# Optimization experiments

Hardware: AMD Instinct MI355X
Metric: run time of the kernel (lower is better)

Reference implementation:

```python
import jax, jax.numpy as jnp
import numpy as np

B, T, IN_DIM = 64, 128, 64
T_ENC, HID, ATTN, OUT = 256, 512, 256, 64


def setup_inputs() -> dict:
    key = jax.random.key(0)
    ks = jax.random.split(key, 12)
    s = lambda *sh: 1.0 / np.sqrt(sh[-1])
    inp = {
        "x": jax.random.normal(ks[0], (B, T, IN_DIM), jnp.float32),
        "encoder_outputs": jax.random.normal(ks[1], (B, T_ENC, HID), jnp.float32),
        # Bahdanau attention params (Linear, no bias): weight shape (out, in)
        "W_query": jax.random.normal(ks[2], (ATTN, HID), jnp.float32) * s(ATTN, HID),
        "W_key": jax.random.normal(ks[3], (ATTN, HID), jnp.float32) * s(ATTN, HID),
        "v": jax.random.normal(ks[4], (1, ATTN), jnp.float32) * s(1, ATTN),
        # LSTM params, PyTorch layout: gates order (i, f, g, o), 4H rows
        "W_ih": jax.random.normal(ks[5], (4 * HID, IN_DIM + HID), jnp.float32) * s(1, HID),
        "W_hh": jax.random.normal(ks[6], (4 * HID, HID), jnp.float32) * s(1, HID),
        "b_ih": jax.random.normal(ks[7], (4 * HID,), jnp.float32) * s(1, HID),
        "b_hh": jax.random.normal(ks[8], (4 * HID,), jnp.float32) * s(1, HID),
        # FC output layer
        "W_fc": jax.random.normal(ks[9], (OUT, HID), jnp.float32) * s(1, HID),
        "b_fc": jax.random.normal(ks[10], (OUT,), jnp.float32) * s(1, HID),
    }
    return inp


def reference(x, encoder_outputs, W_query, W_key, v, W_ih, W_hh, b_ih, b_hh, W_fc, b_fc):
    Bsz = x.shape[0]
    H = W_hh.shape[1]
    # keys projection is constant across timesteps -> hoist out of the loop
    keys_t = jnp.einsum('bed,ad->bea', encoder_outputs, W_key)  # (B, T_enc, A)
    bias = b_ih + b_hh

    def step(carry, x_t):
        h, c = carry  # (B, H) each
        # Bahdanau attention: query = previous top-layer hidden state
        q = jnp.einsum('bh,ah->ba', h, W_query)                 # (B, A)
        energy = jnp.tanh(q[:, None, :] + keys_t)               # (B, T_enc, A)
        e = jnp.einsum('bea,a->be', energy, v[0])               # (B, T_enc)
        w = jax.nn.softmax(e, axis=1)                           # (B, T_enc)
        context = jnp.einsum('be,bed->bd', w, encoder_outputs)  # (B, H)
        # single-step LSTM
        inp = jnp.concatenate([x_t, context], axis=-1)          # (B, IN+H)
        gates = inp @ W_ih.T + h @ W_hh.T + bias                # (B, 4H)
        i_g, f_g, g_g, o_g = jnp.split(gates, 4, axis=-1)
        c_new = jax.nn.sigmoid(f_g) * c + jax.nn.sigmoid(i_g) * jnp.tanh(g_g)
        h_new = jax.nn.sigmoid(o_g) * jnp.tanh(c_new)
        out_t = h_new @ W_fc.T + b_fc                           # (B, OUT)
        return (h_new, c_new), out_t

    h0 = jnp.zeros((Bsz, H), x.dtype)
    c0 = jnp.zeros((Bsz, H), x.dtype)
    _, outs = jax.lax.scan(step, (h0, c0), jnp.swapaxes(x, 0, 1))  # (T, B, OUT)
    return jnp.swapaxes(outs, 0, 1)  # (B, T, OUT)
```

## Files before the change

kernel.cpp:

```cpp
#include <hip/hip_runtime.h>


#define B 64
#define T 128
#define IN_DIM 64
#define TE 256
#define HID 512
#define ATTN 256
#define OUTD 64
#define G 256
#define BS 512

typedef __attribute__((ext_vector_type(8))) short short8;
typedef __attribute__((ext_vector_type(4))) float f32x4;

__device__ __forceinline__ float fast_exp(float x) {
  return __builtin_amdgcn_exp2f(x * 1.44269504f);
}
__device__ __forceinline__ float fast_tanh(float x) {
  float ax = fabsf(x);
  float z = __builtin_amdgcn_exp2f(ax * -2.885390082f);
  float r = (1.f - z) * __builtin_amdgcn_rcpf(1.f + z);
  return copysignf(r, x);
}
__device__ __forceinline__ float fast_sig(float x) {
  float z = __builtin_amdgcn_exp2f(x * -1.44269504f);
  return __builtin_amdgcn_rcpf(1.f + z);
}
__device__ __forceinline__ float bfu(unsigned short u) {
  return __uint_as_float((unsigned)u << 16);
}
__device__ __forceinline__ float bflo(unsigned u) { return __uint_as_float(u << 16); }
__device__ __forceinline__ float bfhi(unsigned u) {
  return __uint_as_float(u & 0xffff0000u);
}
__device__ __forceinline__ unsigned f2bf(float f) {
  unsigned u = __float_as_uint(f);
  return (u + 0x7fff + ((u >> 16) & 1)) >> 16;
}

__device__ __forceinline__ float ald(const float* p) {
  return __hip_atomic_load((float*)p, __ATOMIC_RELAXED, __HIP_MEMORY_SCOPE_AGENT);
}
__device__ __forceinline__ float2 ald2(const float* p) {
  double d = __hip_atomic_load((const double*)p, __ATOMIC_RELAXED,
                               __HIP_MEMORY_SCOPE_AGENT);
  union { double d; float2 f; } u; u.d = d; return u.f;
}
__device__ __forceinline__ unsigned aldu(const unsigned* p) {
  return __hip_atomic_load(p, __ATOMIC_RELAXED, __HIP_MEMORY_SCOPE_AGENT);
}
__device__ __forceinline__ void ast(float* p, float v) {
  __hip_atomic_store(p, v, __ATOMIC_RELAXED, __HIP_MEMORY_SCOPE_AGENT);
}
__device__ __forceinline__ void astu(unsigned* p, unsigned v) {
  __hip_atomic_store(p, v, __ATOMIC_RELAXED, __HIP_MEMORY_SCOPE_AGENT);
}

__device__ __forceinline__ void gridbar(int* flags, int seq, int bid, int tid) {
  asm volatile("s_waitcnt vmcnt(0)" ::: "memory");
  __syncthreads();
  if (tid == 0)
    __hip_atomic_store(&flags[bid], seq, __ATOMIC_RELAXED, __HIP_MEMORY_SCOPE_AGENT);
  if (tid < 64) {
    int* fb = flags + (bid & ~63);
    while (__hip_atomic_load(&fb[tid], __ATOMIC_RELAXED,
                             __HIP_MEMORY_SCOPE_AGENT) < seq) {
      __builtin_amdgcn_s_sleep(1);
    }
  }
  __syncthreads();
}

__global__ void cvt_kernel(const float* __restrict__ src,
                           unsigned short* __restrict__ dst, int n) {
  for (int i = blockIdx.x * blockDim.x + threadIdx.x; i < n;
       i += gridDim.x * blockDim.x)
    dst[i] = (unsigned short)f2bf(src[i]);
}
__global__ void pack2_kernel(const float* __restrict__ src,
                             unsigned* __restrict__ dst, int n2) {
  for (int i = blockIdx.x * blockDim.x + threadIdx.x; i < n2;
       i += gridDim.x * blockDim.x)
    dst[i] = f2bf(src[2 * i]) | (f2bf(src[2 * i + 1]) << 16);
}

__global__ __launch_bounds__(256, 2) void keys_kernel(
    const float* __restrict__ enc, const float* __restrict__ Wk,
    unsigned short* __restrict__ keys2) {
  __shared__ float et[16][512];
  __shared__ float wk[32][256];
  const int tid = threadIdx.x;
  const int b = blockIdx.x >> 4;
  const int e0 = (blockIdx.x & 15) * 16;

  for (int p = 0; p < 8; ++p) {
    int i = p * 256 + tid;
    int e = i >> 7, kq = i & 127;
    float4 vv = *(const float4*)&enc[((size_t)(b * TE + e0 + e)) * HID + kq * 4];
    *(float4*)&et[e][kq * 4] = vv;
  }

  float acc[8][2];
  #pragma unroll
  for (int i = 0; i < 8; ++i) { acc[i][0] = 0.f; acc[i][1] = 0.f; }
  const int a0 = tid & 127;
  const int eh = (tid >> 7) * 8;

  for (int kc = 0; kc < 512; kc += 32) {
    __syncthreads();
    for (int p = 0; p < 8; ++p) {
      int i = p * 256 + tid;
      int a = i >> 3, j4 = (i & 7) * 4;
      float4 w4 = *(const float4*)&Wk[(size_t)a * HID + kc + j4];
      wk[j4 + 0][a] = w4.x; wk[j4 + 1][a] = w4.y;
      wk[j4 + 2][a] = w4.z; wk[j4 + 3][a] = w4.w;
    }
    __syncthreads();
    for (int k = 0; k < 32; ++k) {
      float w0 = wk[k][a0], w1 = wk[k][a0 + 128];
      #pragma unroll
      for (int i = 0; i < 8; ++i) {
        float ev = et[eh + i][kc + k];
        acc[i][0] = fmaf(ev, w0, acc[i][0]);
        acc[i][1] = fmaf(ev, w1, acc[i][1]);
      }
    }
  }
  #pragma unroll
  for (int i = 0; i < 8; ++i)
    #pragma unroll
    for (int h = 0; h < 2; ++h)
      keys2[((size_t)(b * TE + e0 + eh + i)) * ATTN + a0 + 128 * h] =
          (unsigned short)f2bf(acc[i][h]);
}

__global__ __launch_bounds__(BS, 2) void main_kernel(
    const float* __restrict__ v,
    const float* __restrict__ Wih, const float* __restrict__ Whh,
    const float* __restrict__ bih, const float* __restrict__ bhh,
    const float* __restrict__ bfc,
    const unsigned short* __restrict__ enc2, const unsigned short* __restrict__ keys2,
    const unsigned short* __restrict__ Wq2, const unsigned short* __restrict__ Wfc2,
    const unsigned* __restrict__ x2pk,
    float* hbuf, float* cbuf, float* ctxb, float* denb, unsigned* hpk,
    int* flags, float* out) {
  const int bid = blockIdx.x, tid = threadIdx.x;
  const int g = bid >> 6, idx = bid & 63;
  const int b = g * 16 + (idx >> 2), qt = idx & 3;
  const int rg = idx, bg = g;
  const int lane = tid & 63, wv = tid >> 6;

  __shared__ unsigned alds[34 * 256];
  __shared__ float pc[2 * 4 * 16 * 17];
  __shared__ float glds[16 * 33];
  __shared__ float hsh[HID];
  __shared__ float qsh[320];
  __shared__ float lwsh[64];
  __shared__ float dsh[16];
  __shared__ float blds[32];

  if (tid < 32) {
    const int gr2 = (tid >> 3) * 512 + rg * 8 + (tid & 7);
    blds[tid] = bih[gr2] + bhh[gr2];
  }
  const float4 vvf = *(const float4*)&v[lane * 4];
  float kkf[8][4];
  #pragma unroll
  for (int i = 0; i < 8; ++i) {
    const unsigned short* kr =
        keys2 + ((size_t)(b * TE) + qt * 64 + wv * 8 + i) * ATTN + lane * 4;
    uint2 k4 = *(const uint2*)kr;
    kkf[i][0] = bflo(k4.x); kkf[i][1] = bfhi(k4.x);
    kkf[i][2] = bflo(k4.y); kkf[i][3] = bfhi(k4.y);
  }
  const int mL = lane & 15, qL = lane >> 4;
  const int nt = wv >> 2, kq = wv & 3;
  const int kstart = (kq < 2) ? kq * 9 : 18 + (kq - 2) * 8;
  const int nch = (kq < 2) ? 9 : 8;
  const int aoff = mL * 16 + ((qL * 4) ^ (((mL >> 1) & 3) * 4));
  short8 bh[9], bl[9];
  {
    const int rloc = nt * 16 + mL;
    const int grow2 = (rloc >> 3) * 512 + rg * 8 + (rloc & 7);
    #pragma unroll
    for (int c = 0; c < 9; ++c) {
      unsigned uh[4] = {0, 0, 0, 0}, ul[4] = {0, 0, 0, 0};
      if (c < nch) {
        const int kc = kstart + c;
        #pragma unroll
        for (int j = 0; j < 8; ++j) {
          const int k = kc * 32 + qL * 8 + j;
          const float w = (k < 576) ? Wih[(size_t)grow2 * 576 + k]
                                    : Whh[(size_t)grow2 * 512 + (k - 576)];
          const unsigned hi = f2bf(w);
          const float lo = w - __uint_as_float(hi << 16);
          uh[j >> 1] |= hi << (16 * (j & 1));
          ul[j >> 1] |= f2bf(lo) << (16 * (j & 1));
        }
      }
      uint4 th; th.x = uh[0]; th.y = uh[1]; th.z = uh[2]; th.w = uh[3];
      uint4 tl; tl.x = ul[0]; tl.y = ul[1]; tl.z = ul[2]; tl.w = ul[3];
      bh[c] = __builtin_bit_cast(short8, th);
      bl[c] = __builtin_bit_cast(short8, tl);
    }
  }

  const int sm = tid >> 5, ss = tid & 31;
  const int bgl = bg * 16 + sm;
  const int dcol = (ss & 15) ^ (((sm >> 1) & 3) * 4);

  int seq = 0;

  for (int t = 0; t < T; ++t) {
    {
      const float* hprev = hbuf + (size_t)(t & 1) * B * HID;
      hsh[tid] = ald(hprev + (size_t)b * HID + tid);
      {
        unsigned pkx = x2pk[((size_t)bgl * T + t) * 32 + ss];
        const unsigned* hpkc = hpk + (size_t)(t & 1) * B * 256 + (size_t)bgl * 256;
        unsigned ph[8];
        #pragma unroll
        for (int p = 0; p < 8; ++p) ph[p] = aldu(hpkc + ss + 32 * p);
        alds[(ss >> 4) * 256 + sm * 16 + dcol] = pkx;
        #pragma unroll
        for (int p = 0; p < 8; ++p) {
          const int i = ss + 32 * (p + 9);
          alds[(i >> 4) * 256 + sm * 16 + dcol] = ph[p];
        }
      }
      __syncthreads();
      if (t >= 1 && tid < 128) {
        const int o = qt * 16 + (tid >> 3), c = tid & 7;
        const unsigned short* wr = Wfc2 + (size_t)o * HID;
        float oa = 0.f;
        #pragma unroll
        for (int j = 0; j < 8; ++j) {
          const int jj = c * 64 + ((j + c) & 7) * 8;
          uint4 w8 = *(const uint4*)(wr + jj);
          const float* hp = &hsh[jj];
          oa = fmaf(bflo(w8.x), hp[0], oa); oa = fmaf(bfhi(w8.x), hp[1], oa);
          oa = fmaf(bflo(w8.y), hp[2], oa); oa = fmaf(bfhi(w8.y), hp[3], oa);
          oa = fmaf(bflo(w8.z), hp[4], oa); oa = fmaf(bfhi(w8.z), hp[5], oa);
          oa = fmaf(bflo(w8.w), hp[6], oa); oa = fmaf(bfhi(w8.w), hp[7], oa);
        }
        oa += __shfl_xor(oa, 1, 64); oa += __shfl_xor(oa, 2, 64);
        oa += __shfl_xor(oa, 4, 64);
        if (c == 0) out[((size_t)b * T + (t - 1)) * OUTD + o] = oa + bfc[o];
      }
      {
        const int r = tid >> 1, c2 = tid & 1;
        const unsigned short* wr = Wq2 + (size_t)r * HID + c2 * 256;
        const float* hb = &hsh[c2 * 256];
        float qa0 = 0.f, qa1 = 0.f;
        #pragma unroll 8
        for (int j = 0; j < 32; ++j) {
          uint4 w8 = ((const uint4*)wr)[j];
          const float* hp = hb + j * 8;
          qa0 = fmaf(bflo(w8.x), hp[0], qa0); qa0 = fmaf(bfhi(w8.x), hp[1], qa0);
          qa0 = fmaf(bflo(w8.y), hp[2], qa0); qa0 = fmaf(bfhi(w8.y), hp[3], qa0);
          qa1 = fmaf(bflo(w8.z), hp[4], qa1); qa1 = fmaf(bfhi(w8.z), hp[5], qa1);
          qa1 = fmaf(bflo(w8.w), hp[6], qa1); qa1 = fmaf(bfhi(w8.w), hp[7], qa1);
        }
        float qa = qa0 + qa1;
        qa += __shfl_xor(qa, 1, 64);
        if (c2 == 0) qsh[r + (r >> 2)] = qa;
      }
      __syncthreads();
      {
        float q4[4];
        #pragma unroll
        for (int j = 0; j < 4; ++j) q4[j] = qsh[5 * lane + j];
        #pragma unroll
        for (int i = 0; i < 8; ++i) {
          float p = fast_tanh(q4[0] + kkf[i][0]) * vvf.x;
          p = fmaf(fast_tanh(q4[1] + kkf[i][1]), vvf.y, p);
          p = fmaf(fast_tanh(q4[2] + kkf[i][2]), vvf.z, p);
          p = fmaf(fast_tanh(q4[3] + kkf[i][3]), vvf.w, p);
          #pragma unroll
          for (int m = 1; m < 64; m <<= 1) p += __shfl_xor(p, m, 64);
          if (lane == 0) lwsh[wv * 8 + i] = fast_exp(p);
        }
      }
      __syncthreads();
      if (tid < 64) {
        float p = lwsh[tid];
        #pragma unroll
        for (int m = 1; m < 64; m <<= 1) p += __shfl_xor(p, m, 64);
        if (tid == 0) atomicAdd(denb + (t & 1) * B + b, p);
      }
      if (tid < 128)
        ast(ctxb + (size_t)((t + 1) & 1) * B * HID + b * HID + qt * 128 + tid, 0.f);
      if (qt == 0 && tid == 0) ast(denb + ((t + 1) & 1) * B + b, 0.f);
      {
        const unsigned short* erow = enc2 + ((size_t)(b * TE) + qt * 64) * HID + tid;
        float a0 = 0.f, a1 = 0.f, a2 = 0.f, a3 = 0.f;
        #pragma unroll
        for (int e = 0; e < 64; e += 4) {
          a0 = fmaf(lwsh[e],     bfu(erow[(size_t)e * HID]),       a0);
          a1 = fmaf(lwsh[e + 1], bfu(erow[(size_t)(e + 1) * HID]), a1);
          a2 = fmaf(lwsh[e + 2], bfu(erow[(size_t)(e + 2) * HID]), a2);
          a3 = fmaf(lwsh[e + 3], bfu(erow[(size_t)(e + 3) * HID]), a3);
        }
        atomicAdd(ctxb + (size_t)(t & 1) * B * HID + b * HID + tid,
                  (a0 + a1) + (a2 + a3));
      }
    }
    ++seq; gridbar(flags, seq, bid, tid);

    {
      float* hnext = hbuf + (size_t)((t + 1) & 1) * B * HID;
      const float* ctxcur = ctxb + (size_t)(t & 1) * B * HID;
      if (tid < 16) dsh[tid] = ald(denb + (t & 1) * B + bg * 16 + tid);
      float2 cv[8];
      #pragma unroll
      for (int p = 0; p < 8; ++p)
        cv[p] = ald2(ctxcur + (size_t)bgl * HID + (2 * (ss + 32 * (p + 1)) - 64));
      __syncthreads();
      {
        const float li = __builtin_amdgcn_rcpf(dsh[sm]);
        #pragma unroll
        for (int p = 0; p < 8; ++p) {
          const int i = ss + 32 * (p + 1);
          unsigned pk = f2bf(cv[p].x * li) | (f2bf(cv[p].y * li) << 16);
          alds[(i >> 4) * 256 + sm * 16 + dcol] = pk;
        }
      }
      __syncthreads();
      {
        f32x4 ach = {0.f, 0.f, 0.f, 0.f}, acl = {0.f, 0.f, 0.f, 0.f};
        #pragma unroll
        for (int c = 0; c < 9; ++c) {
          if (c < nch) {
            const uint4 av = *(const uint4*)&alds[(kstart + c) * 256 + aoff];
            const short8 a8 = __builtin_bit_cast(short8, av);
            ach = __builtin_amdgcn_mfma_f32_16x16x32_bf16(a8, bh[c], ach, 0, 0, 0);
            acl = __builtin_amdgcn_mfma_f32_16x16x32_bf16(a8, bl[c], acl, 0, 0, 0);
          }
        }
        #pragma unroll
        for (int rr = 0; rr < 4; ++rr)
          pc[((nt * 4 + kq) * 16 + qL * 4 + rr) * 17 + mL] = ach[rr] + acl[rr];
      }
      __syncthreads();
      {
        const int r2 = tid >> 4, mb = tid & 15;
        const int pbase = ((r2 >> 4) * 64 + mb) * 17 + (r2 & 15);
        float s = blds[r2] + ((pc[pbase] + pc[pbase + 272]) +
                              (pc[pbase + 544] + pc[pbase + 816]));
        glds[mb * 33 + r2] = s;
      }
      __syncthreads();
      if (tid < 128) {
        const int bbl = tid >> 3, hl = tid & 7;
        const int bb2 = bg * 16 + bbl, hu = rg * 8 + hl;
        const float gi = glds[bbl * 33 + hl],      gf = glds[bbl * 33 + 8 + hl];
        const float gg = glds[bbl * 33 + 16 + hl], go = glds[bbl * 33 + 24 + hl];
        const float cold = cbuf[bb2 * HID + hu];
        const float cn = fast_sig(gf) * cold + fast_sig(gi) * fast_tanh(gg);
        const float hn = fast_sig(go) * fast_tanh(cn);
        cbuf[bb2 * HID + hu] = cn;
        ast(&hnext[bb2 * HID + hu], hn);
        const float ho = __shfl_xor(hn, 1, 64);
        if ((hl & 1) == 0)
          astu(hpk + (size_t)((t + 1) & 1) * B * 256 + bb2 * 256 + rg * 4 + (hl >> 1),
               f2bf(hn) | (f2bf(ho) << 16));
      }
    }
    ++seq; gridbar(flags, seq, bid, tid);
  }

  {
    hsh[tid] = ald(hbuf + (size_t)b * HID + tid);
    __syncthreads();
    if (tid < 128) {
      const int o = qt * 16 + (tid >> 3), c = tid & 7;
      const unsigned short* wr = Wfc2 + (size_t)o * HID;
      float oa = 0.f;
      #pragma unroll
      for (int j = 0; j < 8; ++j) {
        const int jj = c * 64 + ((j + c) & 7) * 8;
        uint4 w8 = *(const uint4*)(wr + jj);
        const float* hp = &hsh[jj];
        oa = fmaf(bflo(w8.x), hp[0], oa); oa = fmaf(bfhi(w8.x), hp[1], oa);
        oa = fmaf(bflo(w8.y), hp[2], oa); oa = fmaf(bfhi(w8.y), hp[3], oa);
        oa = fmaf(bflo(w8.z), hp[4], oa); oa = fmaf(bfhi(w8.z), hp[5], oa);
        oa = fmaf(bflo(w8.w), hp[6], oa); oa = fmaf(bfhi(w8.w), hp[7], oa);
      }
      oa += __shfl_xor(oa, 1, 64); oa += __shfl_xor(oa, 2, 64);
      oa += __shfl_xor(oa, 4, 64);
      if (c == 0) out[((size_t)b * T + 127) * OUTD + o] = oa + bfc[o];
    }
  }
}

extern "C" void kernel_launch(void* const* d_in, const int* in_sizes, int n_in,
                              void* d_out, int out_size, void* d_ws, size_t ws_size,
                              hipStream_t stream) {
  const float* x   = (const float*)d_in[0];
  const float* enc = (const float*)d_in[1];
  const float* Wq  = (const float*)d_in[2];
  const float* Wk  = (const float*)d_in[3];
  const float* v   = (const float*)d_in[4];
  const float* Wih = (const float*)d_in[5];
  const float* Whh = (const float*)d_in[6];
  const float* bih = (const float*)d_in[7];
  const float* bhh = (const float*)d_in[8];
  const float* Wfc = (const float*)d_in[9];
  const float* bfc = (const float*)d_in[10];

  unsigned short* enc2  = (unsigned short*)d_ws;
  unsigned short* keys2 = enc2 + (size_t)B * TE * HID;
  unsigned short* Wq2   = keys2 + (size_t)B * TE * ATTN;
  unsigned short* Wfc2  = Wq2 + ATTN * HID;
  float* hbuf = (float*)(Wfc2 + OUTD * HID);
  float* cbuf = hbuf + 2 * B * HID;
  float* ctxb = cbuf + B * HID;
  float* denb = ctxb + 2 * B * HID;
  unsigned* hpk = (unsigned*)(denb + 2 * B);
  int* flags = (int*)(hpk + 2 * B * 256);
  unsigned* x2pk = (unsigned*)(flags + 256);

  const size_t zero_units = 2 * B * HID + B * HID + 2 * B * HID + 2 * B +
                            2 * B * 256 + 256;
  hipMemsetAsync(hbuf, 0, zero_units * 4, stream);

  cvt_kernel<<<dim3(512), dim3(256), 0, stream>>>(enc, enc2, B * TE * HID);
  cvt_kernel<<<dim3(64), dim3(256), 0, stream>>>(Wq, Wq2, ATTN * HID);
  cvt_kernel<<<dim3(32), dim3(256), 0, stream>>>(Wfc, Wfc2, OUTD * HID);
  pack2_kernel<<<dim3(128), dim3(256), 0, stream>>>(x, x2pk, B * T * 32);
  keys_kernel<<<dim3(1024), dim3(256), 0, stream>>>(enc, Wk, keys2);
  main_kernel<<<dim3(G), dim3(BS), 0, stream>>>(
      v, Wih, Whh, bih, bhh, bfc, enc2, keys2, Wq2, Wfc2, x2pk,
      hbuf, cbuf, ctxb, denb, hpk, flags, (float*)d_out);
}
```

Measured before the change: 3.322 ms.

## Split query projection across the four blocks of each batch row via flag exchange

Each of the four blocks serving a batch row used to compute the full 256-wide query projection redundantly. Now each block computes only its 64 rows, keeping its Wq slice in registers, writes them to a global exchange buffer, and raises a per-block flag. The other blocks of the row spin on those flags before reading the whole query. This removes 4x redundant Wq reads and FMAs per step, in exchange for an extra inter-block sync, more register pressure (launch bounds changed to waves_per_eu 2), and relaxed-atomic ordering that must be correct.

```diff
diff --git a/kernel.cpp b/kernel.cpp
--- a/kernel.cpp
+++ b/kernel.cpp
@@ -135,7 +135,8 @@
           (unsigned short)f2bf(acc[i][h]);
 }
 
-__global__ __launch_bounds__(BS, 2) void main_kernel(
+__global__ __launch_bounds__(BS, 1) __attribute__((amdgpu_waves_per_eu(2)))
+void main_kernel(
     const float* __restrict__ v,
     const float* __restrict__ Wih, const float* __restrict__ Whh,
     const float* __restrict__ bih, const float* __restrict__ bhh,
@@ -144,7 +145,7 @@
     const unsigned short* __restrict__ Wq2, const unsigned short* __restrict__ Wfc2,
     const unsigned* __restrict__ x2pk,
     float* hbuf, float* cbuf, float* ctxb, float* denb, unsigned* hpk,
-    int* flags, float* out) {
+    int* flags, int* qflag, float* qex, float* out) {
   const int bid = blockIdx.x, tid = threadIdx.x;
   const int g = bid >> 6, idx = bid & 63;
   const int b = g * 16 + (idx >> 2), qt = idx & 3;
@@ -173,6 +174,14 @@
     uint2 k4 = *(const uint2*)kr;
     kkf[i][0] = bflo(k4.x); kkf[i][1] = bfhi(k4.x);
     kkf[i][2] = bflo(k4.y); kkf[i][3] = bfhi(k4.y);
+  }
+  const int qrow = qt * 64 + (tid >> 3);
+  const int qg = tid & 7;
+  unsigned wqr[32];
+  {
+    const unsigned* wqd = (const unsigned*)(Wq2 + (size_t)qrow * HID) + qg * 32;
+    #pragma unroll
+    for (int jj = 0; jj < 32; ++jj) wqr[jj] = wqd[(jj + 2 * qg) & 31];
   }
   const int mL = lane & 15, qL = lane >> 4;
   const int nt = wv >> 2, kq = wv & 3;
@@ -230,6 +239,25 @@
         }
       }
       __syncthreads();
+      {
+        const float* hb = &hsh[qg * 64];
+        float qa0 = 0.f, qa1 = 0.f;
+        #pragma unroll
+        for (int jj = 0; jj < 32; ++jj) {
+          const int kp = ((jj + 2 * qg) & 31) * 2;
+          qa0 = fmaf(bflo(wqr[jj]), hb[kp], qa0);
+          qa1 = fmaf(bfhi(wqr[jj]), hb[kp + 1], qa1);
+        }
+        float qa = qa0 + qa1;
+        qa += __shfl_xor(qa, 1, 64); qa += __shfl_xor(qa, 2, 64);
+        qa += __shfl_xor(qa, 4, 64);
+        if (qg == 0) ast(qex + (size_t)b * 256 + qrow, qa);
+      }
+      asm volatile("s_waitcnt vmcnt(0)" ::: "memory");
+      __syncthreads();
+      if (tid == 0)
+        __hip_atomic_store(&qflag[b * 4 + qt], t + 1, __ATOMIC_RELAXED,
+                           __HIP_MEMORY_SCOPE_AGENT);
       if (t >= 1 && tid < 128) {
         const int o = qt * 16 + (tid >> 3), c = tid & 7;
         const unsigned short* wr = Wfc2 + (size_t)o * HID;
@@ -248,24 +276,17 @@
         oa += __shfl_xor(oa, 4, 64);
         if (c == 0) out[((size_t)b * T + (t - 1)) * OUTD + o] = oa + bfc[o];
       }
-      {
-        const int r = tid >> 1, c2 = tid & 1;
-        const unsigned short* wr = Wq2 + (size_t)r * HID + c2 * 256;
-        const float* hb = &hsh[c2 * 256];
-        float qa0 = 0.f, qa1 = 0.f;
-        #pragma unroll 8
-        for (int j = 0; j < 32; ++j) {
-          uint4 w8 = ((const uint4*)wr)[j];
-          const float* hp = hb + j * 8;
-          qa0 = fmaf(bflo(w8.x), hp[0], qa0); qa0 = fmaf(bfhi(w8.x), hp[1], qa0);
-          qa0 = fmaf(bflo(w8.y), hp[2], qa0); qa0 = fmaf(bfhi(w8.y), hp[3], qa0);
-          qa1 = fmaf(bflo(w8.z), hp[4], qa1); qa1 = fmaf(bfhi(w8.z), hp[5], qa1);
-          qa1 = fmaf(bflo(w8.w), hp[6], qa1); qa1 = fmaf(bfhi(w8.w), hp[7], qa1);
-        }
-        float qa = qa0 + qa1;
-        qa += __shfl_xor(qa, 1, 64);
-        if (c2 == 0) qsh[r + (r >> 2)] = qa;
-      }
+      if (tid < 128)
+        ast(ctxb + (size_t)((t + 1) & 1) * B * HID + b * HID + qt * 128 + tid, 0.f);
+      if (qt == 0 && tid == 0) ast(denb + ((t + 1) & 1) * B + b, 0.f);
+      if (tid < 4 && tid != qt) {
+        while (__hip_atomic_load(&qflag[b * 4 + tid], __ATOMIC_RELAXED,
+                                 __HIP_MEMORY_SCOPE_AGENT) < t + 1) {
+          __builtin_amdgcn_s_sleep(1);
+        }
+      }
+      __syncthreads();
+      if (tid < 256) qsh[tid + (tid >> 2)] = ald(qex + (size_t)b * 256 + tid);
       __syncthreads();
       {
         float q4[4];
@@ -289,9 +310,6 @@
         for (int m = 1; m < 64; m <<= 1) p += __shfl_xor(p, m, 64);
         if (tid == 0) atomicAdd(denb + (t & 1) * B + b, p);
       }
-      if (tid < 128)
-        ast(ctxb + (size_t)((t + 1) & 1) * B * HID + b * HID + qt * 128 + tid, 0.f);
-      if (qt == 0 && tid == 0) ast(denb + ((t + 1) & 1) * B + b, 0.f);
       {
         const unsigned short* erow = enc2 + ((size_t)(b * TE) + qt * 64) * HID + tid;
         float a0 = 0.f, a1 = 0.f, a2 = 0.f, a3 = 0.f;
@@ -419,10 +437,12 @@
   float* denb = ctxb + 2 * B * HID;
   unsigned* hpk = (unsigned*)(denb + 2 * B);
   int* flags = (int*)(hpk + 2 * B * 256);
-  unsigned* x2pk = (unsigned*)(flags + 256);
+  int* qflag = flags + 256;
+  unsigned* x2pk = (unsigned*)(qflag + 256);
+  float* qex = (float*)(x2pk + (size_t)B * T * 32);
 
   const size_t zero_units = 2 * B * HID + B * HID + 2 * B * HID + 2 * B +
-                            2 * B * 256 + 256;
+                            2 * B * 256 + 256 + 256;
   hipMemsetAsync(hbuf, 0, zero_units * 4, stream);
 
   cvt_kernel<<<dim3(512), dim3(256), 0, stream>>>(enc, enc2, B * TE * HID);
@@ -432,5 +452,5 @@
   keys_kernel<<<dim3(1024), dim3(256), 0, stream>>>(enc, Wk, keys2);
   main_kernel<<<dim3(G), dim3(BS), 0, stream>>>(
       v, Wih, Whh, bih, bhh, bfc, enc2, keys2, Wq2, Wfc2, x2pk,
-      hbuf, cbuf, ctxb, denb, hpk, flags, (float*)d_out);
-}
+      hbuf, cbuf, ctxb, denb, hpk, flags, qflag, qex, (float*)d_out);
+}
```

Result: slower. 7.098 ms (+113.6%).
